# Kernel tuning notes

Hardware: AMD Instinct MI355X
Metric: run time of the kernel (lower is better)

Reference implementation:

```python
import jax, jax.numpy as jnp
import numpy as np

HID_GNN = 64
HID_LSTM = 128
FUTURE = 24
N_HYDRO = 32
N_METEO = 64
B, T, E = 32, 168, 384
SLOPE = 0.01  # F.leaky_relu default


def setup_inputs() -> dict:
    key = jax.random.key(0)
    ks = jax.random.split(key, 12)
    N = N_HYDRO + N_METEO
    data_meteo = jax.random.normal(ks[0], (B, T, N_METEO, 1), jnp.float32)
    data_hydro = jax.random.normal(ks[1], (B, T, N_HYDRO, 1), jnp.float32)
    edge_index = jax.random.randint(ks[2], (2, E), 0, N, dtype=jnp.int64)
    # GraphConv(1, HID_GNN): out = lin_root(x) + lin_rel(sum_j x_j) + bias
    W_root = jax.random.normal(ks[3], (HID_GNN, 1), jnp.float32) * 1.0
    W_rel = jax.random.normal(ks[4], (HID_GNN, 1), jnp.float32) * 1.0
    b_gnn = jnp.zeros((HID_GNN,), jnp.float32)
    # Per-station LSTM weights (torch gate order i,f,g,o), stacked over stations
    sih = 1.0 / np.sqrt(HID_GNN)
    shh = 1.0 / np.sqrt(HID_LSTM)
    Wih = jax.random.normal(ks[5], (N_HYDRO, 4 * HID_LSTM, HID_GNN), jnp.float32) * sih
    Whh = jax.random.normal(ks[6], (N_HYDRO, 4 * HID_LSTM, HID_LSTM), jnp.float32) * shh
    bih = jnp.zeros((N_HYDRO, 4 * HID_LSTM), jnp.float32)
    bhh = jnp.zeros((N_HYDRO, 4 * HID_LSTM), jnp.float32)
    W_lin = jax.random.normal(ks[7], (FUTURE, HID_LSTM), jnp.float32) * shh
    b_lin = jnp.zeros((FUTURE,), jnp.float32)
    return {"data_meteo": data_meteo, "data_hydro": data_hydro, "edge_index": edge_index,
            "W_root": W_root, "W_rel": W_rel, "b_gnn": b_gnn,
            "Wih": Wih, "Whh": Whh, "bih": bih, "bhh": bhh,
            "W_lin": W_lin, "b_lin": b_lin}


def _lstm_last(xs, Wih_s, Whh_s, b_s):
    # xs: [B,T,D]; one station's LSTM; returns last hidden [B,H]
    H = Whh_s.shape[1]
    h0 = jnp.zeros((xs.shape[0], H), xs.dtype)

    def step(carry, xt):
        h, c = carry
        gates = xt @ Wih_s.T + h @ Whh_s.T + b_s  # [B,4H]
        i, f, g, o = jnp.split(gates, 4, axis=-1)
        c = jax.nn.sigmoid(f) * c + jax.nn.sigmoid(i) * jnp.tanh(g)
        h = jax.nn.sigmoid(o) * jnp.tanh(c)
        return (h, c), None

    (hT, _), _ = jax.lax.scan(step, (h0, h0), jnp.swapaxes(xs, 0, 1))
    return hT


def reference(data_meteo, data_hydro, edge_index, W_root, W_rel, b_gnn,
              Wih, Whh, bih, bhh, W_lin, b_lin):
    Bn, Tn, Nh, F = data_hydro.shape
    Nm = data_meteo.shape[2]
    N = Nh + Nm
    # [B,T,N,1] -> one graph per (b,t); same edge_index in every graph
    x = jnp.concatenate([data_hydro, data_meteo], axis=2).reshape(Bn * Tn, N, F)
    src, dst = edge_index[0], edge_index[1]
    agg = jnp.zeros_like(x).at[:, dst].add(x[:, src])  # sum aggregation
    h = x @ W_root.T + agg @ W_rel.T + b_gnn          # GraphConv, [G,N,HID_GNN]
    h = jax.nn.leaky_relu(h, SLOPE)
    hydro = h.reshape(Bn, Tn, N, -1)[:, :, :Nh, :]    # [B,T,Nh,HID_GNN]
    # per-station LSTM: vmap over station axis with station-specific weights
    last = jax.vmap(_lstm_last, in_axes=(2, 0, 0, 0))(hydro, Wih, Whh, bih + bhh)  # [Nh,B,H]
    pred = last @ W_lin.T + b_lin                     # [Nh,B,FUTURE]
    pred = jnp.swapaxes(pred, 0, 1)                   # [B,Nh,FUTURE]
    return jax.nn.leaky_relu(pred, SLOPE)
```

## Files before the change

### kernel.cpp

```cpp
#include <hip/hip_runtime.h>

typedef unsigned short u16;
typedef unsigned int u32;
typedef __attribute__((ext_vector_type(8))) short short8;
typedef __attribute__((ext_vector_type(4))) float floatx4;
typedef __attribute__((ext_vector_type(4))) float float4v;

#define B_ 32
#define T_ 168
#define NH_ 32
#define NM_ 64
#define E_ 384
#define HL_ 128
#define FUT_ 24
#define SLOPE_ 0.01f
#define XP_ 80
#define HP_ 144
#define WIH_LP 72
#define WHH_LP 136
#define OVL_E (T_ * 4 * XP_)

#define NS1_ (-1.4426950408889634f)
#define S2_ (2.8853900817779268f)

static __device__ __forceinline__ float b2f(u16 u) {
  u32 v = ((u32)u) << 16;
  return __builtin_bit_cast(float, v);
}
static __device__ __forceinline__ u16 f2bf(float f) {
  u32 x = __builtin_bit_cast(u32, f);
  u32 r = (x + 0x7fffu + ((x >> 16) & 1u)) >> 16;
  return (u16)r;
}
static __device__ __forceinline__ float fexp2(float x) { return __builtin_amdgcn_exp2f(x); }
static __device__ __forceinline__ float frcp(float x) { return __builtin_amdgcn_rcpf(x); }
static __device__ __forceinline__ float sel4(floatx4 v, int r) {
  float m0 = (r & 1) ? v[1] : v[0];
  float m1 = (r & 1) ? v[3] : v[2];
  return (r & 2) ? m1 : m0;
}
static __device__ __forceinline__ float lrelu(float x) { return fmaxf(x, SLOPE_ * x); }

__launch_bounds__(512, 2)
__global__ void fused_kernel(const float* __restrict__ dm, const float* __restrict__ dh,
                             const int* __restrict__ eidx,
                             const float* __restrict__ Wroot, const float* __restrict__ Wrel,
                             const float* __restrict__ bgnn,
                             const float* __restrict__ Wih, const float* __restrict__ Whh,
                             const float* __restrict__ bih, const float* __restrict__ bhh,
                             const float* __restrict__ Wlin, const float* __restrict__ blin,
                             float* __restrict__ out) {
  const int s = blockIdx.x & 31;
  const int bg = blockIdx.x >> 5;
  const int tid = threadIdx.x;
  const int w = tid >> 6;
  const int lane = tid & 63;
  const int cm = lane & 15;
  const int q = lane >> 4;
  const int b = cm & 3;
  const int rho = cm >> 2;

  __shared__ __align__(16) u16 ovl[OVL_E];
  __shared__ __align__(16) u16 hbuf[2 * 4 * HP_];
  __shared__ float xh_lds[4][T_];
  __shared__ float ag_lds[4][T_];
  __shared__ float wr_s[64], wv_s[64], bg_s[64];
  __shared__ int srcs[E_];
  __shared__ int nsrc, iflag;

  if (tid == 0) { nsrc = 0; iflag = 0; }
  for (int i = tid; i < 2 * 4 * HP_; i += 512) hbuf[i] = 0;
  __syncthreads();

  {
    int odd = 0;
    for (int e = tid; e < E_; e += 512) odd |= eidx[2 * e + 1];
    if (odd) atomicOr(&iflag, 1);
  }
  __syncthreads();
  const bool i32 = iflag != 0;

  for (int e = tid; e < E_; e += 512) {
    int se = i32 ? eidx[e] : eidx[2 * e];
    int de = i32 ? eidx[E_ + e] : eidx[2 * E_ + 2 * e];
    if (de == s) { int i = atomicAdd(&nsrc, 1); srcs[i] = se; }
  }
  if (tid < 64) { wr_s[tid] = Wroot[tid]; wv_s[tid] = Wrel[tid]; bg_s[tid] = bgnn[tid]; }
  for (int i = tid; i < 4 * T_; i += 512) {
    int bb = i / T_, t = i % T_;
    xh_lds[bb][t] = dh[((size_t)(bg * 4 + bb) * T_ + t) * NH_ + s];
  }
  floatx4 bias_init[4];
#pragma unroll
  for (int blk = 0; blk < 4; blk++) {
    const float scb = (blk == 2) ? S2_ : NS1_;
#pragma unroll
    for (int r = 0; r < 4; r++) {
      const int nb = blk * 128 + w * 16 + q * 4 + r;
      bias_init[blk][r] = (bih[s * 512 + nb] + bhh[s * 512 + nb]) * scb;
    }
  }
  __syncthreads();

  const int ns = nsrc;
  for (int i = tid; i < 4 * T_; i += 512) {
    int bb = i / T_, t = i % T_;
    size_t gb = (size_t)(bg * 4 + bb) * T_ + t;
    float a = 0.f;
    for (int j = 0; j < ns; j++) {
      int sr = srcs[j];
      a += (sr < NH_) ? dh[gb * NH_ + sr] : dm[gb * NM_ + (sr - NH_)];
    }
    ag_lds[bb][t] = a;
  }

  short8 Af[4][6];
  const int nl = w * 16 + cm;
  __syncthreads();
  {
    const float* g = Wih + (size_t)s * 512 * 64;
#pragma unroll
    for (int it = 0; it < 16; it++) {
      int j = tid + it * 512;
      float4v v = *(const float4v*)(g + 4 * j);
      const float sc = ((j >> 11) == 2) ? S2_ : NS1_;
      u16* dst = ovl + (j >> 4) * WIH_LP + (j & 15) * 4;
      dst[0] = f2bf(v[0] * sc); dst[1] = f2bf(v[1] * sc);
      dst[2] = f2bf(v[2] * sc); dst[3] = f2bf(v[3] * sc);
    }
  }
  __syncthreads();
#pragma unroll
  for (int blk = 0; blk < 4; blk++)
#pragma unroll
    for (int kk = 0; kk < 2; kk++)
      Af[blk][kk] = *(const short8*)(ovl + (blk * 128 + nl) * WIH_LP + kk * 32 + q * 8);
  __syncthreads();
  {
    const float* g = Whh + (size_t)s * 512 * 128;
#pragma unroll
    for (int it = 0; it < 16; it++) {
      int j = tid + it * 512;
      float4v v = *(const float4v*)(g + 4 * j);
      u16* dst = ovl + (j >> 5) * WHH_LP + (j & 31) * 4;
      dst[0] = f2bf(v[0] * NS1_); dst[1] = f2bf(v[1] * NS1_);
      dst[2] = f2bf(v[2] * NS1_); dst[3] = f2bf(v[3] * NS1_);
    }
  }
  __syncthreads();
#pragma unroll
  for (int blk = 0; blk < 2; blk++)
#pragma unroll
    for (int kk = 0; kk < 4; kk++)
      Af[blk][2 + kk] = *(const short8*)(ovl + (blk * 128 + nl) * WHH_LP + kk * 32 + q * 8);
  __syncthreads();
  {
    const float* g = Whh + ((size_t)s * 512 + 256) * 128;
#pragma unroll
    for (int it = 0; it < 16; it++) {
      int j = tid + it * 512;
      float4v v = *(const float4v*)(g + 4 * j);
      const float sc = (j < 4096) ? S2_ : NS1_;
      u16* dst = ovl + (j >> 5) * WHH_LP + (j & 31) * 4;
      dst[0] = f2bf(v[0] * sc); dst[1] = f2bf(v[1] * sc);
      dst[2] = f2bf(v[2] * sc); dst[3] = f2bf(v[3] * sc);
    }
  }
  __syncthreads();
#pragma unroll
  for (int blk = 2; blk < 4; blk++)
#pragma unroll
    for (int kk = 0; kk < 4; kk++)
      Af[blk][2 + kk] = *(const short8*)(ovl + ((blk - 2) * 128 + nl) * WHH_LP + kk * 32 + q * 8);
  __syncthreads();

  {
    const int k = tid & 63;
    const int bb = (tid >> 6) & 3;
    const int th = tid >> 8;
    const float wrk = wr_s[k], wvk = wv_s[k], bgk = bg_s[k];
    for (int i = 0; i < T_ / 2; i++) {
      const int t = th * (T_ / 2) + i;
      const float xv = xh_lds[bb][t] * wrk + ag_lds[bb][t] * wvk + bgk;
      ovl[t * (4 * XP_) + bb * XP_ + k] = f2bf(lrelu(xv));
    }
  }
  __syncthreads();

  floatx4 accN[4];
  {
    short8 Bx0 = *(const short8*)(ovl + b * XP_ + q * 8);
    short8 Bx1 = *(const short8*)(ovl + b * XP_ + 32 + q * 8);
#pragma unroll
    for (int blk = 0; blk < 4; blk++) {
      accN[blk] = __builtin_amdgcn_mfma_f32_16x16x32_bf16(Af[blk][0], Bx0, bias_init[blk], 0, 0, 0);
      accN[blk] = __builtin_amdgcn_mfma_f32_16x16x32_bf16(Af[blk][1], Bx1, accN[blk], 0, 0, 0);
    }
  }
  float c = 0.0f;
#pragma unroll 2
  for (int t = 0; t < T_; t++) {
    const int p = t & 1, pn = p ^ 1;
    short8 Bh[4];
#pragma unroll
    for (int kk = 0; kk < 4; kk++)
      Bh[kk] = *(const short8*)(hbuf + p * (4 * HP_) + b * HP_ + kk * 32 + q * 8);
    short8 Bx0n, Bx1n;
    const bool more = (t + 1 < T_);
    if (more) {
      Bx0n = *(const short8*)(ovl + (t + 1) * (4 * XP_) + b * XP_ + q * 8);
      Bx1n = *(const short8*)(ovl + (t + 1) * (4 * XP_) + b * XP_ + 32 + q * 8);
    }

    floatx4 a2 = accN[2], a0 = accN[0];
#pragma unroll
    for (int kk = 0; kk < 4; kk++) {
      a2 = __builtin_amdgcn_mfma_f32_16x16x32_bf16(Af[2][2 + kk], Bh[kk], a2, 0, 0, 0);
      a0 = __builtin_amdgcn_mfma_f32_16x16x32_bf16(Af[0][2 + kk], Bh[kk], a0, 0, 0, 0);
    }
    const float gg = sel4(a2, rho);
    const float gi = sel4(a0, rho);
    const float Eg = fexp2(gg);
    const float Ei = fexp2(gi);

    floatx4 a1 = accN[1], a3 = accN[3];
#pragma unroll
    for (int kk = 0; kk < 4; kk++) {
      a1 = __builtin_amdgcn_mfma_f32_16x16x32_bf16(Af[1][2 + kk], Bh[kk], a1, 0, 0, 0);
      a3 = __builtin_amdgcn_mfma_f32_16x16x32_bf16(Af[3][2 + kk], Bh[kk], a3, 0, 0, 0);
    }
    if (more) {
#pragma unroll
      for (int blk = 0; blk < 4; blk++) {
        accN[blk] = __builtin_amdgcn_mfma_f32_16x16x32_bf16(Af[blk][0], Bx0n, bias_init[blk], 0, 0, 0);
        accN[blk] = __builtin_amdgcn_mfma_f32_16x16x32_bf16(Af[blk][1], Bx1n, accN[blk], 0, 0, 0);
      }
    }

    const float tg = 1.0f - 2.0f * frcp(1.0f + Eg);
    const float si = frcp(1.0f + Ei);
    const float gf = sel4(a1, rho);
    const float go = sel4(a3, rho);
    const float sf = frcp(1.0f + fexp2(gf));
    c = sf * c + si * tg;
    const float tc = 1.0f - 2.0f * frcp(1.0f + fexp2(S2_ * c));
    const float so = frcp(1.0f + fexp2(go));
    const float hh = so * tc;
    u32 pk;
    asm("v_cvt_pk_bf16_f32 %0, %1, %2" : "=v"(pk) : "v"(hh), "v"(hh));
    hbuf[pn * (4 * HP_) + b * HP_ + w * 16 + q * 4 + rho] = (u16)pk;
    __syncthreads();
  }

  if (tid < 4 * FUT_) {
    const int bb = tid / FUT_;
    const int f = tid % FUT_;
    float a = blin[f];
#pragma unroll 8
    for (int k = 0; k < HL_; k++) a += b2f(hbuf[bb * HP_ + k]) * Wlin[f * HL_ + k];
    out[((size_t)(bg * 4 + bb) * NH_ + s) * FUT_ + f] = lrelu(a);
  }
}

extern "C" void kernel_launch(void* const* d_in, const int* in_sizes, int n_in,
                              void* d_out, int out_size, void* d_ws, size_t ws_size,
                              hipStream_t stream) {
  const float* dm = (const float*)d_in[0];
  const float* dh = (const float*)d_in[1];
  const int* eidx = (const int*)d_in[2];
  const float* Wroot = (const float*)d_in[3];
  const float* Wrel = (const float*)d_in[4];
  const float* bgnn = (const float*)d_in[5];
  const float* Wih = (const float*)d_in[6];
  const float* Whh = (const float*)d_in[7];
  const float* bih = (const float*)d_in[8];
  const float* bhh = (const float*)d_in[9];
  const float* Wlin = (const float*)d_in[10];
  const float* blin = (const float*)d_in[11];
  float* out = (float*)d_out;

  fused_kernel<<<256, 512, 0, stream>>>(dm, dh, eidx, Wroot, Wrel, bgnn, Wih, Whh,
                                        bih, bhh, Wlin, blin, out);
}
```

Before: 191.7 us.

## Batch input-gate MFMAs over four timesteps via LDS staging buffer

Each lane's MFMA column covers a different timestep (rho), so the input projections for four timesteps are computed in one MFMA batch every four steps. The results are stashed in a new LDS buffer and read back as a float4 per step. This takes the per-step input MFMAs and their bias chaining off the serial recurrence path. In exchange it adds LDS traffic, a larger shared-memory footprint that may cut occupancy, and the sel4 result now needs an extra add.

```diff
diff --git a/kernel.cpp b/kernel.cpp
--- a/kernel.cpp
+++ b/kernel.cpp
@@ -19,6 +19,9 @@
 #define WIH_LP 72
 #define WHH_LP 136
 #define OVL_E (T_ * 4 * XP_)
+#define XG_B 68
+#define XG_T (4 * XG_B)
+#define XG_W (4 * XG_T)
 
 #define NS1_ (-1.4426950408889634f)
 #define S2_ (2.8853900817779268f)
@@ -62,6 +65,7 @@
 
   __shared__ __align__(16) u16 ovl[OVL_E];
   __shared__ __align__(16) u16 hbuf[2 * 4 * HP_];
+  __shared__ __align__(16) float xgbuf[8 * XG_W];
   __shared__ float xh_lds[4][T_];
   __shared__ float ag_lds[4][T_];
   __shared__ float wr_s[64], wv_s[64], bg_s[64];
@@ -187,69 +191,74 @@
   }
   __syncthreads();
 
-  floatx4 accN[4];
-  {
-    short8 Bx0 = *(const short8*)(ovl + b * XP_ + q * 8);
-    short8 Bx1 = *(const short8*)(ovl + b * XP_ + 32 + q * 8);
-#pragma unroll
-    for (int blk = 0; blk < 4; blk++) {
-      accN[blk] = __builtin_amdgcn_mfma_f32_16x16x32_bf16(Af[blk][0], Bx0, bias_init[blk], 0, 0, 0);
-      accN[blk] = __builtin_amdgcn_mfma_f32_16x16x32_bf16(Af[blk][1], Bx1, accN[blk], 0, 0, 0);
-    }
-  }
+  floatx4 zvec;
+  zvec[0] = 0.f; zvec[1] = 0.f; zvec[2] = 0.f; zvec[3] = 0.f;
+  float* const xgw = xgbuf + w * XG_W + rho * XG_T + b * XG_B + q * 16;
+  const float* const xgr = xgbuf + w * XG_W + b * XG_B + q * 16 + rho * 4;
+
   float c = 0.0f;
-#pragma unroll 2
-  for (int t = 0; t < T_; t++) {
-    const int p = t & 1, pn = p ^ 1;
-    short8 Bh[4];
-#pragma unroll
-    for (int kk = 0; kk < 4; kk++)
-      Bh[kk] = *(const short8*)(hbuf + p * (4 * HP_) + b * HP_ + kk * 32 + q * 8);
-    short8 Bx0n, Bx1n;
-    const bool more = (t + 1 < T_);
-    if (more) {
-      Bx0n = *(const short8*)(ovl + (t + 1) * (4 * XP_) + b * XP_ + q * 8);
-      Bx1n = *(const short8*)(ovl + (t + 1) * (4 * XP_) + b * XP_ + 32 + q * 8);
-    }
-
-    floatx4 a2 = accN[2], a0 = accN[0];
-#pragma unroll
-    for (int kk = 0; kk < 4; kk++) {
-      a2 = __builtin_amdgcn_mfma_f32_16x16x32_bf16(Af[2][2 + kk], Bh[kk], a2, 0, 0, 0);
-      a0 = __builtin_amdgcn_mfma_f32_16x16x32_bf16(Af[0][2 + kk], Bh[kk], a0, 0, 0, 0);
-    }
-    const float gg = sel4(a2, rho);
-    const float gi = sel4(a0, rho);
-    const float Eg = fexp2(gg);
-    const float Ei = fexp2(gi);
-
-    floatx4 a1 = accN[1], a3 = accN[3];
-#pragma unroll
-    for (int kk = 0; kk < 4; kk++) {
-      a1 = __builtin_amdgcn_mfma_f32_16x16x32_bf16(Af[1][2 + kk], Bh[kk], a1, 0, 0, 0);
-      a3 = __builtin_amdgcn_mfma_f32_16x16x32_bf16(Af[3][2 + kk], Bh[kk], a3, 0, 0, 0);
-    }
-    if (more) {
+  for (int tt = 0; tt < T_ / 4; tt++) {
+    {
+      const int tb = tt * 4 + rho;
+      short8 Bx0 = *(const short8*)(ovl + tb * (4 * XP_) + b * XP_ + q * 8);
+      short8 Bx1 = *(const short8*)(ovl + tb * (4 * XP_) + b * XP_ + 32 + q * 8);
+      floatx4 ax[4];
 #pragma unroll
       for (int blk = 0; blk < 4; blk++) {
-        accN[blk] = __builtin_amdgcn_mfma_f32_16x16x32_bf16(Af[blk][0], Bx0n, bias_init[blk], 0, 0, 0);
-        accN[blk] = __builtin_amdgcn_mfma_f32_16x16x32_bf16(Af[blk][1], Bx1n, accN[blk], 0, 0, 0);
-      }
-    }
-
-    const float tg = 1.0f - 2.0f * frcp(1.0f + Eg);
-    const float si = frcp(1.0f + Ei);
-    const float gf = sel4(a1, rho);
-    const float go = sel4(a3, rho);
-    const float sf = frcp(1.0f + fexp2(gf));
-    c = sf * c + si * tg;
-    const float tc = 1.0f - 2.0f * frcp(1.0f + fexp2(S2_ * c));
-    const float so = frcp(1.0f + fexp2(go));
-    const float hh = so * tc;
-    u32 pk;
-    asm("v_cvt_pk_bf16_f32 %0, %1, %2" : "=v"(pk) : "v"(hh), "v"(hh));
-    hbuf[pn * (4 * HP_) + b * HP_ + w * 16 + q * 4 + rho] = (u16)pk;
-    __syncthreads();
+        ax[blk] = __builtin_amdgcn_mfma_f32_16x16x32_bf16(Af[blk][0], Bx0, bias_init[blk], 0, 0, 0);
+        ax[blk] = __builtin_amdgcn_mfma_f32_16x16x32_bf16(Af[blk][1], Bx1, ax[blk], 0, 0, 0);
+      }
+#pragma unroll
+      for (int r = 0; r < 4; r++) {
+        floatx4 vv;
+        vv[0] = ax[0][r]; vv[1] = ax[1][r]; vv[2] = ax[2][r]; vv[3] = ax[3][r];
+        *(floatx4*)(xgw + r * 4) = vv;
+      }
+    }
+
+#pragma unroll
+    for (int u = 0; u < 4; u++) {
+      const int p = u & 1, pn = p ^ 1;
+      short8 Bh[4];
+#pragma unroll
+      for (int kk = 0; kk < 4; kk++)
+        Bh[kk] = *(const short8*)(hbuf + p * (4 * HP_) + b * HP_ + kk * 32 + q * 8);
+      const floatx4 xgv = *(const floatx4*)(xgr + u * XG_T);
+
+      floatx4 a2 = __builtin_amdgcn_mfma_f32_16x16x32_bf16(Af[2][2], Bh[0], zvec, 0, 0, 0);
+      floatx4 a0 = __builtin_amdgcn_mfma_f32_16x16x32_bf16(Af[0][2], Bh[0], zvec, 0, 0, 0);
+#pragma unroll
+      for (int kk = 1; kk < 4; kk++) {
+        a2 = __builtin_amdgcn_mfma_f32_16x16x32_bf16(Af[2][2 + kk], Bh[kk], a2, 0, 0, 0);
+        a0 = __builtin_amdgcn_mfma_f32_16x16x32_bf16(Af[0][2 + kk], Bh[kk], a0, 0, 0, 0);
+      }
+      const float gg = sel4(a2, rho) + xgv[2];
+      const float gi = sel4(a0, rho) + xgv[0];
+      const float Eg = fexp2(gg);
+      const float Ei = fexp2(gi);
+
+      floatx4 a1 = __builtin_amdgcn_mfma_f32_16x16x32_bf16(Af[1][2], Bh[0], zvec, 0, 0, 0);
+      floatx4 a3 = __builtin_amdgcn_mfma_f32_16x16x32_bf16(Af[3][2], Bh[0], zvec, 0, 0, 0);
+#pragma unroll
+      for (int kk = 1; kk < 4; kk++) {
+        a1 = __builtin_amdgcn_mfma_f32_16x16x32_bf16(Af[1][2 + kk], Bh[kk], a1, 0, 0, 0);
+        a3 = __builtin_amdgcn_mfma_f32_16x16x32_bf16(Af[3][2 + kk], Bh[kk], a3, 0, 0, 0);
+      }
+
+      const float tg = 1.0f - 2.0f * frcp(1.0f + Eg);
+      const float si = frcp(1.0f + Ei);
+      const float gf = sel4(a1, rho) + xgv[1];
+      const float go = sel4(a3, rho) + xgv[3];
+      const float sf = frcp(1.0f + fexp2(gf));
+      c = sf * c + si * tg;
+      const float tc = 1.0f - 2.0f * frcp(1.0f + fexp2(S2_ * c));
+      const float so = frcp(1.0f + fexp2(go));
+      const float hh = so * tc;
+      u32 pk;
+      asm("v_cvt_pk_bf16_f32 %0, %1, %2" : "=v"(pk) : "v"(hh), "v"(hh));
+      hbuf[pn * (4 * HP_) + b * HP_ + w * 16 + q * 4 + rho] = (u16)pk;
+      __syncthreads();
+    }
   }
 
   if (tid < 4 * FUT_) {
```

New measurement: 179.7 us. -6.2%, faster.
